# Performance work log

Measured on AMD Instinct MI355X. Metric: run time of the kernel, lower is better.

Reference implementation:

```python
import jax, jax.numpy as jnp
import numpy as np

B, S, D, H, FF = 2, 2048, 1024, 16, 4096
DH = D // H
EPS = 1e-5


def rmsnorm(x, g):
    rms = jnp.sqrt(jnp.mean(x * x, axis=-1, keepdims=True) + EPS)
    return x / rms * g


def gelu(x):
    return x * 0.5 * (1.0 + jax.lax.erf(x / np.float32(np.sqrt(2.0))))


def setup_inputs() -> dict:
    key = jax.random.key(0)
    ks = jax.random.split(key, 9)
    sd = np.float32(1.0 / np.sqrt(D))
    sf = np.float32(1.0 / np.sqrt(FF))
    return {
        'x': jax.random.normal(ks[0], (B, S, D), jnp.float32),
        'wq': jax.random.normal(ks[1], (D, D), jnp.float32) * sd,
        'wk': jax.random.normal(ks[2], (D, D), jnp.float32) * sd,
        'wv': jax.random.normal(ks[3], (D, D), jnp.float32) * sd,
        'wo': jax.random.normal(ks[4], (D, D), jnp.float32) * sd,
        'w1': jax.random.normal(ks[5], (FF, D), jnp.float32) * sd,
        'w2': jax.random.normal(ks[6], (D, FF), jnp.float32) * sf,
        'g1': jax.random.uniform(ks[7], (D,), jnp.float32),
        'g2': jax.random.uniform(ks[8], (D,), jnp.float32),
    }


def reference(x, wq, wk, wv, wo, w1, w2, g1, g2):
    b, s, d = x.shape
    h = rmsnorm(x, g1)
    # torch Linear: y = x @ W.T ; split heads -> [b, s, H, DH]
    q = jnp.einsum('bsd,ed->bse', h, wq).reshape(b, s, H, DH)
    k = jnp.einsum('bsd,ed->bse', h, wk).reshape(b, s, H, DH)
    v = jnp.einsum('bsd,ed->bse', h, wv).reshape(b, s, H, DH)
    score = jnp.einsum('bqhd,bkhd->bhqk', q, k) / np.float32(np.sqrt(DH))
    causal = jnp.triu(jnp.ones((s, s), bool), 1)  # strictly upper = masked
    score = score + jnp.where(causal, jnp.float32(-1e9), jnp.float32(0.0))
    attn_w = jax.nn.softmax(score, axis=-1)
    o = jnp.einsum('bhqk,bkhd->bqhd', attn_w, v).reshape(b, s, d)
    attn_out = jnp.einsum('bsd,ed->bse', o, wo)
    x2 = attn_out + x
    h2 = rmsnorm(x2, g2)
    ffn = jnp.einsum('bsf,df->bsd', gelu(jnp.einsum('bsd,fd->bsf', h2, w1)), w2)
    return ffn + x2
```

## Files before the change

### kernel.cpp

```cpp
#include <hip/hip_runtime.h>
#include <cstdint>

#define B_ 2
#define S_ 2048
#define D_ 1024
#define H_ 16
#define DH_ 64
#define FF_ 4096
#define M_TOK (B_ * S_)

typedef __attribute__((ext_vector_type(8))) short short8;
typedef __attribute__((ext_vector_type(4))) float f32x4;
typedef __attribute__((ext_vector_type(4))) unsigned short us4;

typedef unsigned short u16;

#define SCL 0.18033688011112042f

__device__ __forceinline__ float bf2f(u16 u) {
  union { uint32_t u; float f; } x;
  x.u = ((uint32_t)u) << 16;
  return x.f;
}
__device__ __forceinline__ u16 f2bf(float f) {
  union { float f; uint32_t u; } x;
  x.f = f;
  uint32_t r = x.u + 0x7FFFu + ((x.u >> 16) & 1u);
  return (u16)(r >> 16);
}

__device__ __forceinline__ void gl_lds16(const void* g, void* l) {
  __builtin_amdgcn_global_load_lds(
      (const __attribute__((address_space(1))) uint32_t*)(uintptr_t)g,
      (__attribute__((address_space(3))) uint32_t*)(uintptr_t)l, 16, 0, 0);
}

__device__ __forceinline__ float gelu_f(float v) {
  const float y = 0.7978845608f * (v + 0.044715f * v * v * v);
  const float t = exp2f(y * 2.885390082f);
  const float th = 1.0f - 2.0f * __builtin_amdgcn_rcpf(t + 1.0f);
  return 0.5f * v * (1.0f + th);
}

#define MEG 1048576
__global__ __launch_bounds__(256) void cvt_all_k(const float* __restrict__ wq, const float* __restrict__ wk,
                                                 const float* __restrict__ wv, const float* __restrict__ wo,
                                                 const float* __restrict__ w1, const float* __restrict__ w2,
                                                 u16* __restrict__ wqkv, u16* __restrict__ wob,
                                                 u16* __restrict__ w1b, u16* __restrict__ w2b) {
  const int n = (blockIdx.x * 256 + threadIdx.x) * 4;
  const float* src;
  u16* dst;
  int off;
  if (n < 3 * MEG) {
    dst = wqkv; off = n;
    src = (n < MEG) ? wq + n : (n < 2 * MEG ? wk + (n - MEG) : wv + (n - 2 * MEG));
  } else if (n < 4 * MEG) {
    dst = wob; off = n - 3 * MEG; src = wo + off;
  } else if (n < 8 * MEG) {
    dst = w1b; off = n - 4 * MEG; src = w1 + off;
  } else {
    dst = w2b; off = n - 8 * MEG; src = w2 + off;
  }
  const float4 v = *(const float4*)src;
  us4 o;
  o[0] = f2bf(v.x); o[1] = f2bf(v.y); o[2] = f2bf(v.z); o[3] = f2bf(v.w);
  *(us4*)&dst[off] = o;
}

__global__ __launch_bounds__(256) void zero_k(float* __restrict__ Of, float* __restrict__ L) {
  const int i = (blockIdx.x * 256 + threadIdx.x) * 4;
  if (i < 4 * MEG) { *(float4*)&Of[i] = float4{0.f, 0.f, 0.f, 0.f}; }
  else { *(float4*)&L[i - 4 * MEG] = float4{0.f, 0.f, 0.f, 0.f}; }
}

__global__ __launch_bounds__(256) void norm_o_k(const float* __restrict__ Of, const float* __restrict__ L,
                                                u16* __restrict__ O) {
  const int row = blockIdx.x;
  const int tid = threadIdx.x;
  const int col = tid * 4;
  const int hh = col >> 6;
  const float lv = L[(size_t)((row >> 11) * 16 + hh) * 2048 + (row & 2047)];
  const float inv = 1.0f / lv;
  const float4 v = *(const float4*)&Of[(size_t)row * D_ + col];
  us4 o;
  o[0] = f2bf(v.x * inv); o[1] = f2bf(v.y * inv);
  o[2] = f2bf(v.z * inv); o[3] = f2bf(v.w * inv);
  *(us4*)&O[(size_t)row * D_ + col] = o;
}

__global__ __launch_bounds__(256) void rmsnorm_k(const float* __restrict__ X,
                                                 const float* __restrict__ G,
                                                 u16* __restrict__ Hout) {
  const int row = blockIdx.x;
  const int tid = threadIdx.x;
  const float4 xx = *(const float4*)&X[(size_t)row * D_ + tid * 4];
  float v[4] = {xx.x, xx.y, xx.z, xx.w};
  float s = 0.f;
#pragma unroll
  for (int i = 0; i < 4; ++i) s += v[i] * v[i];
#pragma unroll
  for (int d = 1; d < 64; d <<= 1) s += __shfl_xor(s, d);
  __shared__ float red[4];
  if ((tid & 63) == 0) red[tid >> 6] = s;
  __syncthreads();
  s = red[0] + red[1] + red[2] + red[3];
  const float scale = rsqrtf(s * (1.0f / (float)D_) + 1e-5f);
  const float4 gg = *(const float4*)&G[tid * 4];
  us4 o;
  o[0] = f2bf(v[0] * scale * gg.x);
  o[1] = f2bf(v[1] * scale * gg.y);
  o[2] = f2bf(v[2] * scale * gg.z);
  o[3] = f2bf(v[3] * scale * gg.w);
  *(us4*)&Hout[(size_t)row * D_ + tid * 4] = o;
}

__global__ __launch_bounds__(256) void rmsnorm_wo_k(const u16* __restrict__ P0, const u16* __restrict__ P1,
                                                    const float* __restrict__ X, const float* __restrict__ G,
                                                    float* __restrict__ X2, u16* __restrict__ Hout) {
  const int row = blockIdx.x;
  const int tid = threadIdx.x;
  const size_t off = (size_t)row * D_ + tid * 4;
  const us4 p0 = *(const us4*)&P0[off];
  const us4 p1 = *(const us4*)&P1[off];
  const float4 xx = *(const float4*)&X[off];
  float v[4];
  v[0] = bf2f(p0[0]) + bf2f(p1[0]) + xx.x;
  v[1] = bf2f(p0[1]) + bf2f(p1[1]) + xx.y;
  v[2] = bf2f(p0[2]) + bf2f(p1[2]) + xx.z;
  v[3] = bf2f(p0[3]) + bf2f(p1[3]) + xx.w;
  *(float4*)&X2[off] = float4{v[0], v[1], v[2], v[3]};
  float s = 0.f;
#pragma unroll
  for (int i = 0; i < 4; ++i) s += v[i] * v[i];
#pragma unroll
  for (int d = 1; d < 64; d <<= 1) s += __shfl_xor(s, d);
  __shared__ float red[4];
  if ((tid & 63) == 0) red[tid >> 6] = s;
  __syncthreads();
  s = red[0] + red[1] + red[2] + red[3];
  const float scale = rsqrtf(s * (1.0f / (float)D_) + 1e-5f);
  const float4 gg = *(const float4*)&G[tid * 4];
  us4 o;
  o[0] = f2bf(v[0] * scale * gg.x);
  o[1] = f2bf(v[1] * scale * gg.y);
  o[2] = f2bf(v[2] * scale * gg.z);
  o[3] = f2bf(v[3] * scale * gg.w);
  *(us4*)&Hout[off] = o;
}

__global__ __launch_bounds__(256) void ffn2_red_k(const u16* __restrict__ Q0, const u16* __restrict__ Q1,
                                                  float* __restrict__ OUT) {
  const int i = (blockIdx.x * 256 + threadIdx.x) * 4;
  const us4 a = *(const us4*)&Q0[i];
  const us4 b = *(const us4*)&Q1[i];
  const float4 c = *(const float4*)&OUT[i];
  *(float4*)&OUT[i] = float4{bf2f(a[0]) + bf2f(b[0]) + c.x, bf2f(a[1]) + bf2f(b[1]) + c.y,
                             bf2f(a[2]) + bf2f(b[2]) + c.z, bf2f(a[3]) + bf2f(b[3]) + c.w};
}

template <int MODE>
__global__ __launch_bounds__(256) void gemm_bt_k(const u16* __restrict__ A,
                                                 const u16* __restrict__ W,
                                                 u16* __restrict__ C0, u16* __restrict__ C1,
                                                 u16* __restrict__ C2, int N, int K) {
  __shared__ alignas(16) u16 As[128 * 32];
  __shared__ alignas(16) u16 Bs[128 * 32];
  const int tid = threadIdx.x;
  const int wv = tid >> 6, lane = tid & 63;
  const int r = lane & 15, quad = lane >> 4;
  const int nx = gridDim.x;
  const int nwg = nx * gridDim.y;
  const int orig = blockIdx.x + nx * blockIdx.y;
  const int id = (orig & 7) * (nwg >> 3) + (orig >> 3);
  const int bn = (id % nx) * 128;
  const int bm = (id / nx) * 128;
  const int row0 = (wv >> 1) * 64, col0 = (wv & 1) * 64;

  f32x4 acc[4][4] = {};

  int srow[2], sg[2];
#pragma unroll
  for (int jj = 0; jj < 2; ++jj) {
    const int c = wv * 128 + jj * 64 + lane;
    srow[jj] = c >> 2;
    sg[jj] = (c & 3) ^ ((srow[jj] >> 1) & 3);
  }

  for (int k0 = 0; k0 < K; k0 += 32) {
#pragma unroll
    for (int jj = 0; jj < 2; ++jj) {
      const int l0 = (wv * 128 + jj * 64) * 8;
      gl_lds16(&A[(size_t)(bm + srow[jj]) * K + k0 + sg[jj] * 8], &As[l0]);
      gl_lds16(&W[(size_t)(bn + srow[jj]) * K + k0 + sg[jj] * 8], &Bs[l0]);
    }
    __syncthreads();
    short8 af[4], bf[4];
#pragma unroll
    for (int mt = 0; mt < 4; ++mt) {
      const int mr = row0 + mt * 16 + r;
      af[mt] = *(const short8*)&As[mr * 32 + (quad ^ ((mr >> 1) & 3)) * 8];
    }
#pragma unroll
    for (int nt = 0; nt < 4; ++nt) {
      const int nr = col0 + nt * 16 + r;
      bf[nt] = *(const short8*)&Bs[nr * 32 + (quad ^ ((nr >> 1) & 3)) * 8];
    }
#pragma unroll
    for (int mt = 0; mt < 4; ++mt)
#pragma unroll
      for (int nt = 0; nt < 4; ++nt)
        acc[mt][nt] = __builtin_amdgcn_mfma_f32_16x16x32_bf16(af[mt], bf[nt], acc[mt][nt], 0, 0, 0);
    __syncthreads();
  }

  if constexpr (MODE == 2) {
#pragma unroll
    for (int mt = 0; mt < 4; ++mt)
#pragma unroll
      for (int nt = 0; nt < 4; ++nt)
#pragma unroll
        for (int i = 0; i < 4; ++i) {
          const int grow = bm + row0 + mt * 16 + quad * 4 + i;
          const int gcol = bn + col0 + nt * 16 + r;
          C0[(size_t)grow * N + gcol] = f2bf(gelu_f(acc[mt][nt][i]));
        }
  } else {
    if (bn < 2048) {
#pragma unroll
      for (int mt = 0; mt < 4; ++mt) {
        const int grow0 = bm + row0 + mt * 16 + quad * 4;
#pragma unroll
        for (int nt = 0; nt < 4; ++nt) {
          const int gcol = bn + col0 + nt * 16 + r;
          u16* dst = (gcol < 1024) ? C0 : C1;
          const float sc = (gcol < 1024) ? SCL : 1.0f;
          const int cc = gcol & 1023;
#pragma unroll
          for (int i = 0; i < 4; ++i)
            dst[(size_t)(grow0 + i) * 1024 + cc] = f2bf(acc[mt][nt][i] * sc);
        }
      }
    } else {
#pragma unroll
      for (int mtp = 0; mtp < 4; mtp += 2) {
        const int tok0 = bm + row0 + mtp * 16 + quad * 4;
#pragma unroll
        for (int nt = 0; nt < 4; ++nt) {
          const int vcol = bn + col0 + nt * 16 + r - 2048;
          const size_t vtrow = (size_t)((tok0 >> 11) * 16 + (vcol >> 6)) * 64 + (vcol & 63);
#pragma unroll
          for (int i = 0; i < 4; ++i) {
            const int s = (tok0 + i) & 2047;
            const uint32_t pk =
                (uint32_t)f2bf(acc[mtp][nt][i]) | ((uint32_t)f2bf(acc[mtp + 1][nt][i]) << 16);
            *(uint32_t*)&C2[vtrow * 2048 + s + (s & 15)] = pk;
          }
        }
      }
    }
  }
}

__global__ __launch_bounds__(256) void gemm_sk2_k(const u16* __restrict__ A,
                                                  const u16* __restrict__ W,
                                                  u16* __restrict__ P0, u16* __restrict__ P1,
                                                  int N, int K, int KS) {
  __shared__ alignas(16) u16 As[128 * 32];
  __shared__ alignas(16) u16 Bs[128 * 32];
  const int tid = threadIdx.x;
  const int wv = tid >> 6, lane = tid & 63;
  const int r = lane & 15, quad = lane >> 4;
  const int orig = blockIdx.x + 8 * (blockIdx.y + 32 * blockIdx.z);
  const int id = (orig & 7) * 64 + (orig >> 3);
  const int bn = (id & 7) * 128;
  const int bm = ((id >> 3) & 31) * 128;
  const int bz = id >> 8;
  const int row0 = (wv >> 1) * 64, col0 = (wv & 1) * 64;
  const int koff = bz * KS;
  u16* P = bz ? P1 : P0;

  f32x4 acc[4][4] = {};

  int srow[2], sg[2];
#pragma unroll
  for (int jj = 0; jj < 2; ++jj) {
    const int c = wv * 128 + jj * 64 + lane;
    srow[jj] = c >> 2;
    sg[jj] = (c & 3) ^ ((srow[jj] >> 1) & 3);
  }

  for (int k0 = koff; k0 < koff + KS; k0 += 32) {
#pragma unroll
    for (int jj = 0; jj < 2; ++jj) {
      const int l0 = (wv * 128 + jj * 64) * 8;
      gl_lds16(&A[(size_t)(bm + srow[jj]) * K + k0 + sg[jj] * 8], &As[l0]);
      gl_lds16(&W[(size_t)(bn + srow[jj]) * K + k0 + sg[jj] * 8], &Bs[l0]);
    }
    __syncthreads();
    short8 af[4], bf[4];
#pragma unroll
    for (int mt = 0; mt < 4; ++mt) {
      const int mr = row0 + mt * 16 + r;
      af[mt] = *(const short8*)&As[mr * 32 + (quad ^ ((mr >> 1) & 3)) * 8];
    }
#pragma unroll
    for (int nt = 0; nt < 4; ++nt) {
      const int nr = col0 + nt * 16 + r;
      bf[nt] = *(const short8*)&Bs[nr * 32 + (quad ^ ((nr >> 1) & 3)) * 8];
    }
#pragma unroll
    for (int mt = 0; mt < 4; ++mt)
#pragma unroll
      for (int nt = 0; nt < 4; ++nt)
        acc[mt][nt] = __builtin_amdgcn_mfma_f32_16x16x32_bf16(af[mt], bf[nt], acc[mt][nt], 0, 0, 0);
    __syncthreads();
  }

#pragma unroll
  for (int mt = 0; mt < 4; ++mt)
#pragma unroll
    for (int nt = 0; nt < 4; ++nt)
#pragma unroll
      for (int i = 0; i < 4; ++i) {
        const int grow = bm + row0 + mt * 16 + quad * 4 + i;
        const int gcol = bn + col0 + nt * 16 + r;
        P[(size_t)grow * N + gcol] = f2bf(acc[mt][nt][i]);
      }
}

__global__ __launch_bounds__(256, 2) void attn_k(const u16* __restrict__ Q,
                                                 const u16* __restrict__ Kx,
                                                 const u16* __restrict__ VT,
                                                 float* __restrict__ Of, float* __restrict__ L) {
  __shared__ alignas(16) u16 Ks[2][32 * 72];
  __shared__ alignas(16) u16 Vs[2][64 * 40];
  __shared__ alignas(16) u16 Ps[4][32 * 40];

  const int tid = threadIdx.x;
  const int wv = tid >> 6, lane = tid & 63;
  const int r = lane & 15, quad = lane >> 4;

  const int orig = blockIdx.x + 40 * blockIdx.y;
  const int sid = (orig & 7) * 160 + (orig >> 3);
  const int sx = sid % 40;
  const int bh = sid / 40;
  const int b = bh >> 4, hh = bh & 15;

  int id = 39 - sx;
  int bx = 0;
  for (;;) {
    const int nb = (bx >> 2) + 1;
    if (id < nb) break;
    id -= nb;
    ++bx;
  }
  const int c = id;
  const int j0base = c * 512;
  const int niter = (min(bx * 128 + 128, j0base + 512) - j0base) >> 5;

  const int qbase = bx * 128;
  const int m0 = qbase + wv * 32;
  const size_t base = (size_t)b * S_ * D_ + (size_t)hh * DH_;
  const u16* Qb = Q + base;
  const u16* Kb = Kx + base;
  const u16* VTb = VT + (size_t)bh * 64 * 2048;
  u16* Psw = &Ps[wv][0];

  short8 qf[2][2];
#pragma unroll
  for (int f = 0; f < 2; ++f) {
    qf[f][0] = *(const short8*)&Qb[(size_t)(m0 + f * 16 + r) * D_ + quad * 8];
    qf[f][1] = *(const short8*)&Qb[(size_t)(m0 + f * 16 + r) * D_ + 32 + quad * 8];
  }

  short8 onesv;
#pragma unroll
  for (int e = 0; e < 8; ++e) onesv[e] = (short)0x3F80;

  f32x4 oacc[2][4] = {};
  f32x4 lacc[2] = {};

  const int krow = tid >> 3, kg = tid & 7;
  const int vrow = tid >> 2, vg = tid & 3;

  *(short8*)&Ks[0][krow * 72 + kg * 8] = *(const short8*)&Kb[(size_t)(j0base + krow) * D_ + kg * 8];
  *(short8*)&Vs[0][vrow * 40 + vg * 8] = *(const short8*)&VTb[(size_t)vrow * 2048 + j0base + vg * 8];

  int cur = 0;
  for (int it = 0; it < niter; ++it) {
    const int j0 = j0base + it * 32;
    __syncthreads();

    short8 kreg, vreg;
    const bool pf_next = (it + 1 < niter);
    if (pf_next) {
      const int j1 = j0 + 32;
      kreg = *(const short8*)&Kb[(size_t)(j1 + krow) * D_ + kg * 8];
      vreg = *(const short8*)&VTb[(size_t)vrow * 2048 + j1 + vg * 8];
    }

    f32x4 z[2][2];
    __builtin_amdgcn_s_setprio(1);
#pragma unroll
    for (int kt = 0; kt < 2; ++kt) {
      const short8 kf0 = *(const short8*)&Ks[cur][(kt * 16 + r) * 72 + quad * 8];
      const short8 kf1 = *(const short8*)&Ks[cur][(kt * 16 + r) * 72 + 32 + quad * 8];
#pragma unroll
      for (int f = 0; f < 2; ++f) {
        f32x4 zz = {};
        zz = __builtin_amdgcn_mfma_f32_16x16x32_bf16(qf[f][0], kf0, zz, 0, 0, 0);
        zz = __builtin_amdgcn_mfma_f32_16x16x32_bf16(qf[f][1], kf1, zz, 0, 0, 0);
        z[f][kt] = zz;
      }
    }
    __builtin_amdgcn_s_setprio(0);

    const bool masked = (j0 + 31 > m0);
#pragma unroll
    for (int f = 0; f < 2; ++f)
#pragma unroll
      for (int i = 0; i < 4; ++i) {
        const int qrow = m0 + f * 16 + quad * 4 + i;
        float v0 = z[f][0][i];
        float v1 = z[f][1][i];
        if (masked) {
          if (j0 + r > qrow) v0 = -128.f;
          if (j0 + 16 + r > qrow) v1 = -128.f;
        }
        const uint32_t pk = (uint32_t)f2bf(exp2f(v0)) | ((uint32_t)f2bf(exp2f(v1)) << 16);
        *(uint32_t*)&Psw[(f * 16 + quad * 4 + i) * 40 + r * 2] = pk;
      }

    asm volatile("s_waitcnt lgkmcnt(0)" ::: "memory");

    short8 vf[4];
#pragma unroll
    for (int nt = 0; nt < 4; ++nt)
      vf[nt] = *(const short8*)&Vs[cur][(nt * 16 + r) * 40 + quad * 8];
    __builtin_amdgcn_s_setprio(1);
#pragma unroll
    for (int f = 0; f < 2; ++f) {
      const short8 pf = *(const short8*)&Psw[(f * 16 + r) * 40 + quad * 8];
#pragma unroll
      for (int nt = 0; nt < 4; ++nt)
        oacc[f][nt] = __builtin_amdgcn_mfma_f32_16x16x32_bf16(pf, vf[nt], oacc[f][nt], 0, 0, 0);
      lacc[f] = __builtin_amdgcn_mfma_f32_16x16x32_bf16(pf, onesv, lacc[f], 0, 0, 0);
    }
    __builtin_amdgcn_s_setprio(0);

    if (pf_next) {
      *(short8*)&Ks[cur ^ 1][krow * 72 + kg * 8] = kreg;
      *(short8*)&Vs[cur ^ 1][vrow * 40 + vg * 8] = vreg;
    }

    cur ^= 1;
  }

#pragma unroll
  for (int f = 0; f < 2; ++f) {
#pragma unroll
    for (int i = 0; i < 4; ++i) {
      const int qrow = m0 + f * 16 + quad * 4 + i;
#pragma unroll
      for (int nt = 0; nt < 4; ++nt)
        atomicAdd(&Of[base + (size_t)qrow * D_ + nt * 16 + r], oacc[f][nt][i]);
      if (r == 0) atomicAdd(&L[(size_t)bh * 2048 + qrow], lacc[f][i]);
    }
  }
}

extern "C" void kernel_launch(void* const* d_in, const int* in_sizes, int n_in,
                              void* d_out, int out_size, void* d_ws, size_t ws_size,
                              hipStream_t stream) {
  (void)in_sizes; (void)n_in; (void)out_size; (void)ws_size;
  const float* x   = (const float*)d_in[0];
  const float* wq  = (const float*)d_in[1];
  const float* wk  = (const float*)d_in[2];
  const float* wvp = (const float*)d_in[3];
  const float* wo  = (const float*)d_in[4];
  const float* w1  = (const float*)d_in[5];
  const float* w2  = (const float*)d_in[6];
  const float* g1  = (const float*)d_in[7];
  const float* g2  = (const float*)d_in[8];
  float* out = (float*)d_out;

  u16* ws = (u16*)d_ws;
  const size_t TD = (size_t)M_TOK * D_;
  u16* h    = ws;
  u16* q    = ws + 1 * TD;
  u16* k    = ws + 2 * TD;
  u16* vt   = ws + 3 * TD;
  u16* h2   = ws + 4 * TD;
  float* l  = (float*)(ws + 4 * TD);
  u16* o    = h;
  u16* t    = ws;
  u16* P0   = q;
  u16* P1   = k;
  u16* Q0   = h2;
  u16* wqkv = ws + 5 * TD;
  u16* wob  = wqkv + 3 * MEG;
  u16* w1b  = wob + 1 * MEG;
  u16* w2b  = w1b + 4 * MEG;
  u16* Q1   = w2b + 4 * MEG;

  const dim3 blk(256);

  cvt_all_k<<<12288, blk, 0, stream>>>(wq, wk, wvp, wo, w1, w2, wqkv, wob, w1b, w2b);
  zero_k<<<(4 * MEG + 65536) / 1024, blk, 0, stream>>>(out, l);
  rmsnorm_k<<<M_TOK, blk, 0, stream>>>(x, g1, h);
  gemm_bt_k<4><<<dim3(24, 32), blk, 0, stream>>>(h, wqkv, q, k, vt, 3072, 1024);
  attn_k<<<dim3(40, 32), blk, 0, stream>>>(q, k, vt, out, l);
  norm_o_k<<<M_TOK, blk, 0, stream>>>(out, l, o);
  gemm_sk2_k<<<dim3(8, 32, 2), blk, 0, stream>>>(o, wob, P0, P1, 1024, 1024, 512);
  rmsnorm_wo_k<<<M_TOK, blk, 0, stream>>>(P0, P1, x, g2, out, h2);
  gemm_bt_k<2><<<dim3(32, 32), blk, 0, stream>>>(h2, w1b, t, nullptr, nullptr, 4096, 1024);
  gemm_sk2_k<<<dim3(8, 32, 2), blk, 0, stream>>>(t, w2b, Q0, Q1, 1024, 4096, 2048);
  ffn2_red_k<<<4096, blk, 0, stream>>>(Q0, Q1, out);
}
```

Measured before the change: 374.2 us.

## Deepen attention K/V prefetch to two tiles ahead and unroll loop by two

The attention inner loop is unrolled by two with static LDS buffer indices. Global loads for K/V now run two tiles ahead in register ping-pong, replacing the one-tile-ahead prefetch, so there is more time to hide global load latency. The bf16 packing of exp2 results also becomes a cheaper round-half-up perm-based pack. This adds register pressure and slightly changes rounding (no ties-to-even), and it assumes niter is even and at least 2, since the unconditional second body and the initial prefetch of tile 1 depend on that.

```diff
diff --git a/kernel.cpp b/kernel.cpp
--- a/kernel.cpp
+++ b/kernel.cpp
@@ -27,6 +27,16 @@
   x.f = f;
   uint32_t r = x.u + 0x7FFFu + ((x.u >> 16) & 1u);
   return (u16)(r >> 16);
+}
+
+__device__ __forceinline__ uint32_t pack2bf(float a, float b) {
+  union { float f; uint32_t u; } x, y;
+  x.f = a; y.f = b;
+#if __has_builtin(__builtin_amdgcn_perm)
+  return __builtin_amdgcn_perm(y.u + 0x8000u, x.u + 0x8000u, 0x07060302u);
+#else
+  return ((x.u + 0x8000u) >> 16) | ((y.u + 0x8000u) & 0xFFFF0000u);
+#endif
 }
 
 __device__ __forceinline__ void gl_lds16(const void* g, void* l) {
@@ -329,6 +339,55 @@
       }
 }
 
+#define ATTN_BODY(BUF, J0, RINK, RINV, ROUTK, ROUTV, DO_PF, DO_WR)                                 \
+  {                                                                                                \
+    __syncthreads();                                                                               \
+    if (DO_PF) {                                                                                   \
+      ROUTK = *(const short8*)&Kb[(size_t)((J0) + 64 + krow) * D_ + kg * 8];                       \
+      ROUTV = *(const short8*)&VTb[(size_t)vrow * 2048 + (J0) + 64 + vg * 8];                      \
+    }                                                                                              \
+    f32x4 z[2][2];                                                                                 \
+    __builtin_amdgcn_s_setprio(1);                                                                 \
+    _Pragma("unroll") for (int kt = 0; kt < 2; ++kt) {                                             \
+      const short8 kf0 = *(const short8*)&Ks[BUF][(kt * 16 + r) * 72 + quad * 8];                  \
+      const short8 kf1 = *(const short8*)&Ks[BUF][(kt * 16 + r) * 72 + 32 + quad * 8];             \
+      _Pragma("unroll") for (int f = 0; f < 2; ++f) {                                              \
+        f32x4 zz = {};                                                                             \
+        zz = __builtin_amdgcn_mfma_f32_16x16x32_bf16(qf[f][0], kf0, zz, 0, 0, 0);                  \
+        zz = __builtin_amdgcn_mfma_f32_16x16x32_bf16(qf[f][1], kf1, zz, 0, 0, 0);                  \
+        z[f][kt] = zz;                                                                             \
+      }                                                                                            \
+    }                                                                                              \
+    __builtin_amdgcn_s_setprio(0);                                                                 \
+    const bool masked = ((J0) + 31 > m0);                                                          \
+    _Pragma("unroll") for (int f = 0; f < 2; ++f) _Pragma("unroll") for (int i = 0; i < 4; ++i) {  \
+      const int qrow = m0 + f * 16 + quad * 4 + i;                                                 \
+      float v0 = z[f][0][i];                                                                       \
+      float v1 = z[f][1][i];                                                                       \
+      if (masked) {                                                                                \
+        if ((J0) + r > qrow) v0 = -128.f;                                                          \
+        if ((J0) + 16 + r > qrow) v1 = -128.f;                                                     \
+      }                                                                                            \
+      *(uint32_t*)&Psw[(f * 16 + quad * 4 + i) * 40 + r * 2] = pack2bf(exp2f(v0), exp2f(v1));      \
+    }                                                                                              \
+    asm volatile("s_waitcnt lgkmcnt(0)" ::: "memory");                                             \
+    short8 vf[4];                                                                                  \
+    _Pragma("unroll") for (int nt = 0; nt < 4; ++nt)                                               \
+        vf[nt] = *(const short8*)&Vs[BUF][(nt * 16 + r) * 40 + quad * 8];                          \
+    __builtin_amdgcn_s_setprio(1);                                                                 \
+    _Pragma("unroll") for (int f = 0; f < 2; ++f) {                                                \
+      const short8 pf = *(const short8*)&Psw[(f * 16 + r) * 40 + quad * 8];                        \
+      _Pragma("unroll") for (int nt = 0; nt < 4; ++nt)                                             \
+          oacc[f][nt] = __builtin_amdgcn_mfma_f32_16x16x32_bf16(pf, vf[nt], oacc[f][nt], 0, 0, 0); \
+      lacc[f] = __builtin_amdgcn_mfma_f32_16x16x32_bf16(pf, onesv, lacc[f], 0, 0, 0);              \
+    }                                                                                              \
+    __builtin_amdgcn_s_setprio(0);                                                                 \
+    if (DO_WR) {                                                                                   \
+      *(short8*)&Ks[(BUF) ^ 1][krow * 72 + kg * 8] = RINK;                                         \
+      *(short8*)&Vs[(BUF) ^ 1][vrow * 40 + vg * 8] = RINV;                                         \
+    }                                                                                              \
+  }
+
 __global__ __launch_bounds__(256, 2) void attn_k(const u16* __restrict__ Q,
                                                  const u16* __restrict__ Kx,
                                                  const u16* __restrict__ VT,
@@ -386,75 +445,14 @@
 
   *(short8*)&Ks[0][krow * 72 + kg * 8] = *(const short8*)&Kb[(size_t)(j0base + krow) * D_ + kg * 8];
   *(short8*)&Vs[0][vrow * 40 + vg * 8] = *(const short8*)&VTb[(size_t)vrow * 2048 + j0base + vg * 8];
-
-  int cur = 0;
-  for (int it = 0; it < niter; ++it) {
+  short8 kA, vA, kB, vB;
+  kA = *(const short8*)&Kb[(size_t)(j0base + 32 + krow) * D_ + kg * 8];
+  vA = *(const short8*)&VTb[(size_t)vrow * 2048 + j0base + 32 + vg * 8];
+
+  for (int it = 0; it < niter; it += 2) {
     const int j0 = j0base + it * 32;
-    __syncthreads();
-
-    short8 kreg, vreg;
-    const bool pf_next = (it + 1 < niter);
-    if (pf_next) {
-      const int j1 = j0 + 32;
-      kreg = *(const short8*)&Kb[(size_t)(j1 + krow) * D_ + kg * 8];
-      vreg = *(const short8*)&VTb[(size_t)vrow * 2048 + j1 + vg * 8];
-    }
-
-    f32x4 z[2][2];
-    __builtin_amdgcn_s_setprio(1);
-#pragma unroll
-    for (int kt = 0; kt < 2; ++kt) {
-      const short8 kf0 = *(const short8*)&Ks[cur][(kt * 16 + r) * 72 + quad * 8];
-      const short8 kf1 = *(const short8*)&Ks[cur][(kt * 16 + r) * 72 + 32 + quad * 8];
-#pragma unroll
-      for (int f = 0; f < 2; ++f) {
-        f32x4 zz = {};
-        zz = __builtin_amdgcn_mfma_f32_16x16x32_bf16(qf[f][0], kf0, zz, 0, 0, 0);
-        zz = __builtin_amdgcn_mfma_f32_16x16x32_bf16(qf[f][1], kf1, zz, 0, 0, 0);
-        z[f][kt] = zz;
-      }
-    }
-    __builtin_amdgcn_s_setprio(0);
-
-    const bool masked = (j0 + 31 > m0);
-#pragma unroll
-    for (int f = 0; f < 2; ++f)
-#pragma unroll
-      for (int i = 0; i < 4; ++i) {
-        const int qrow = m0 + f * 16 + quad * 4 + i;
-        float v0 = z[f][0][i];
-        float v1 = z[f][1][i];
-        if (masked) {
-          if (j0 + r > qrow) v0 = -128.f;
-          if (j0 + 16 + r > qrow) v1 = -128.f;
-        }
-        const uint32_t pk = (uint32_t)f2bf(exp2f(v0)) | ((uint32_t)f2bf(exp2f(v1)) << 16);
-        *(uint32_t*)&Psw[(f * 16 + quad * 4 + i) * 40 + r * 2] = pk;
-      }
-
-    asm volatile("s_waitcnt lgkmcnt(0)" ::: "memory");
-
-    short8 vf[4];
-#pragma unroll
-    for (int nt = 0; nt < 4; ++nt)
-      vf[nt] = *(const short8*)&Vs[cur][(nt * 16 + r) * 40 + quad * 8];
-    __builtin_amdgcn_s_setprio(1);
-#pragma unroll
-    for (int f = 0; f < 2; ++f) {
-      const short8 pf = *(const short8*)&Psw[(f * 16 + r) * 40 + quad * 8];
-#pragma unroll
-      for (int nt = 0; nt < 4; ++nt)
-        oacc[f][nt] = __builtin_amdgcn_mfma_f32_16x16x32_bf16(pf, vf[nt], oacc[f][nt], 0, 0, 0);
-      lacc[f] = __builtin_amdgcn_mfma_f32_16x16x32_bf16(pf, onesv, lacc[f], 0, 0, 0);
-    }
-    __builtin_amdgcn_s_setprio(0);
-
-    if (pf_next) {
-      *(short8*)&Ks[cur ^ 1][krow * 72 + kg * 8] = kreg;
-      *(short8*)&Vs[cur ^ 1][vrow * 40 + vg * 8] = vreg;
-    }
-
-    cur ^= 1;
+    ATTN_BODY(0, j0, kA, vA, kB, vB, (it + 2 < niter), true);
+    ATTN_BODY(1, j0 + 32, kB, vB, kA, vA, (it + 3 < niter), (it + 2 < niter));
   }
 
 #pragma unroll
```

After: 367.0 us. Within noise of the previous version (-1.9%).
